# Kernel optimization log

Measured on AMD Instinct MI355X. Metric: run time of the kernel, lower is better.

Reference implementation:

```python
import jax, jax.numpy as jnp
import numpy as np

N, V, D, H, E = 16384, 17, 128, 256, 32
LN_EPS = 1e-5


def setup_inputs() -> dict:
    key = jax.random.key(0)
    ks = jax.random.split(key, 16)
    s = lambda *sh: 1.0 / np.sqrt(sh[0])
    inp = {
        "h": jax.random.normal(ks[0], (N, V, D), dtype=jnp.float32),
        "xy": jax.random.normal(ks[1], (N, V, 2), dtype=jnp.float32),
        "joint_mask": jax.random.randint(ks[2], (N, V), 0, 2).astype(bool),
        "edge_index": jax.random.randint(ks[3], (E, 2), 0, V).astype(jnp.int64),
        # edge MLP: Linear(2D+2 -> H), ReLU, Linear(H -> D)
        "ew1": jax.random.normal(ks[4], (2 * D + 2, H), dtype=jnp.float32) * s(2 * D + 2),
        "eb1": jnp.zeros((H,), dtype=jnp.float32),
        "ew2": jax.random.normal(ks[5], (H, D), dtype=jnp.float32) * s(H),
        "eb2": jnp.zeros((D,), dtype=jnp.float32),
        # node MLP: Linear(2D -> H), ReLU, Linear(H -> D)
        "nw1": jax.random.normal(ks[6], (2 * D, H), dtype=jnp.float32) * s(2 * D),
        "nb1": jnp.zeros((H,), dtype=jnp.float32),
        "nw2": jax.random.normal(ks[7], (H, D), dtype=jnp.float32) * s(H),
        "nb2": jnp.zeros((D,), dtype=jnp.float32),
        # LayerNorm(D)
        "gamma": jnp.ones((D,), dtype=jnp.float32),
        "beta": jnp.zeros((D,), dtype=jnp.float32),
    }
    return inp


def reference(h, xy, joint_mask, edge_index, ew1, eb1, ew2, eb2,
              nw1, nb1, nw2, nb2, gamma, beta):
    dst = edge_index[:, 0]  # [E]
    src = edge_index[:, 1]  # [E]
    mask_f = joint_mask.astype(h.dtype)  # [N,V]

    target = h[:, dst, :]                  # [N,E,D]
    source = h[:, src, :]                  # [N,E,D]
    rel = xy[:, src, :] - xy[:, dst, :]    # [N,E,2]
    edge_valid = (joint_mask[:, dst] & joint_mask[:, src]).astype(h.dtype)  # [N,E]

    msg_in = jnp.concatenate([target, source, rel], axis=-1)  # [N,E,2D+2]
    msg = jax.nn.relu(msg_in @ ew1 + eb1) @ ew2 + eb2          # [N,E,D]
    msg = msg * edge_valid[..., None]

    agg = jnp.zeros_like(h).at[:, dst, :].add(msg)                           # [N,V,D]
    denom = jnp.zeros((h.shape[0], h.shape[1], 1), h.dtype).at[:, dst, :].add(
        edge_valid[..., None])                                               # [N,V,1]
    agg = agg / jnp.maximum(denom, 1.0)

    delta = jax.nn.relu(jnp.concatenate([h, agg], axis=-1) @ nw1 + nb1) @ nw2 + nb2
    has_neighbors = (denom > 0).astype(h.dtype)
    x = h + delta * has_neighbors

    mu = jnp.mean(x, axis=-1, keepdims=True)
    var = jnp.mean(jnp.square(x - mu), axis=-1, keepdims=True)
    out = (x - mu) / jnp.sqrt(var + LN_EPS) * gamma + beta
    return out * mask_f[..., None]
```

## Files before the change

kernel.cpp:

```cpp
#include <hip/hip_runtime.h>

typedef _Float16 half8 __attribute__((ext_vector_type(8)));
typedef _Float16 half4v __attribute__((ext_vector_type(4)));
typedef float f32x4 __attribute__((ext_vector_type(4)));
typedef unsigned int u32;

#define LDH 136

__global__ void prep_weights(const float* __restrict__ ew1,
                             const float* __restrict__ ew2,
                             const float* __restrict__ nw1,
                             const float* __restrict__ nw2,
                             _Float16* __restrict__ wz) {
  int o = blockIdx.x * 256 + threadIdx.x;
  if (o < 65536) {
    int s = o >> 12, r = o & 4095;
    int gs = r >> 9, lane = (r >> 3) & 63, j = r & 7;
    int k = ((s & 1) * 4 + (gs >> 1)) * 32 + (lane >> 4) * 8 + j;
    int n = (s >> 1) * 32 + (gs & 1) * 16 + (lane & 15);
    wz[o] = (_Float16)ew1[k * 256 + n];
  } else if (o < 98304) {
    int o2 = o - 65536;
    int nc = o2 >> 12, r = o2 & 4095;
    int nt2 = r >> 9, lane = (r >> 3) & 63, j = r & 7;
    int k = nc * 32 + (lane >> 4) * 8 + j;
    int n = nt2 * 16 + (lane & 15);
    wz[o] = (_Float16)ew2[k * 128 + n];
  } else if (o < 163840) {
    int o2 = o - 98304;
    int s = o2 >> 12, r = o2 & 4095;
    int gs = r >> 9, lane = (r >> 3) & 63, j = r & 7;
    int k = ((s & 1) * 4 + (gs >> 1)) * 32 + (lane >> 4) * 8 + j;
    int n = (s >> 1) * 32 + (gs & 1) * 16 + (lane & 15);
    wz[o] = (_Float16)nw1[k * 256 + n];
  } else if (o < 196608) {
    int o2 = o - 163840;
    int nc = o2 >> 12, r = o2 & 4095;
    int nt2 = r >> 9, lane = (r >> 3) & 63, j = r & 7;
    int k = nc * 32 + (lane >> 4) * 8 + j;
    int n = nt2 * 16 + (lane & 15);
    wz[o] = (_Float16)nw2[k * 128 + n];
  }
}

__global__ __launch_bounds__(256, 2)
void fused_graph_layer(const float* __restrict__ h, const float* __restrict__ xy,
                       const int* __restrict__ jmask, const int* __restrict__ eidx,
                       const float* __restrict__ ew1,
                       const float* __restrict__ eb1, const float* __restrict__ eb2,
                       const float* __restrict__ nb1, const float* __restrict__ nb2,
                       const float* __restrict__ gamma, const float* __restrict__ beta,
                       const _Float16* __restrict__ wz,
                       float* __restrict__ out) {
  __shared__ _Float16 sh_h16[68 * LDH];
  __shared__ _Float16 sh_agg16[68 * LDH] __attribute__((aligned(16)));
  __shared__ _Float16 sh_ws[4 * 1280];
  __shared__ float sh_rel[256];
  __shared__ float sh_valid[128];
  __shared__ float sh_dn[80];
  __shared__ float sh_hasn[68], sh_maskf[68];
  __shared__ int   sh_edge[64];

  const int tid  = threadIdx.x;
  const int wave = tid >> 6;
  const int lane = tid & 63;
  const int ln   = lane & 15;
  const int quad = lane >> 4;
  const int n0   = blockIdx.x * 4;
  const size_t hbase = (size_t)n0 * 2176;
  const f32x4 vzero = {0.f, 0.f, 0.f, 0.f};

  _Float16* ws = sh_ws + wave * 1280;

  const _Float16* w1img  = wz;
  const _Float16* w2img  = wz + 65536;
  const _Float16* nw1img = wz + 98304;
  const _Float16* nw2img = wz + 163840;
  const float* w1r0 = ew1 + 256 * 256;
  const float* w1r1 = ew1 + 257 * 256;

  if (tid < 64) sh_edge[tid] = eidx[tid];
  if (tid < 68) sh_maskf[tid] = (float)jmask[n0 * 17 + tid];
  for (int i = tid; i < 2176; i += 256) {
    const float4 hv = ((const float4*)(h + hbase))[i];
    int q = i << 2;
    int gv = q >> 7, d = q & 127;
    half4v hq = { (_Float16)hv.x, (_Float16)hv.y, (_Float16)hv.z, (_Float16)hv.w };
    *(half4v*)&sh_h16[gv * LDH + d] = hq;
  }
  __syncthreads();
  if (tid < 128) {
    int g = tid >> 5, e = tid & 31;
    int dv = sh_edge[2 * e], sv = sh_edge[2 * e + 1];
    const float* xyb = xy + (size_t)(n0 + g) * 34;
    sh_rel[2 * tid]     = xyb[2 * sv]     - xyb[2 * dv];
    sh_rel[2 * tid + 1] = xyb[2 * sv + 1] - xyb[2 * dv + 1];
    sh_valid[tid] = sh_maskf[g * 17 + dv] * sh_maskf[g * 17 + sv];
  }
  __syncthreads();

  if (lane < 17) {
    float den = 0.f;
    for (int e = 0; e < 32; ++e)
      den += (sh_edge[2 * e] == lane) ? sh_valid[wave * 32 + e] : 0.f;
    sh_dn[wave * 20 + lane] = den;
    sh_hasn[wave * 17 + lane] = den > 0.f ? 1.f : 0.f;
  }

  int baseT[2], baseS[2];
  #pragma unroll
  for (int mi = 0; mi < 2; ++mi) {
    int eL = mi * 16 + ln;
    baseT[mi] = (wave * 17 + sh_edge[2 * eL]) * LDH;
    baseS[mi] = (wave * 17 + sh_edge[2 * eL + 1]) * LDH;
  }
  half8 af[2][8];
  #pragma unroll
  for (int mi = 0; mi < 2; ++mi)
    #pragma unroll
    for (int ks = 0; ks < 8; ++ks)
      af[mi][ks] = (ks < 4)
          ? *(const half8*)&sh_h16[baseT[mi] + ks * 32 + quad * 8]
          : *(const half8*)&sh_h16[baseS[mi] + (ks - 4) * 32 + quad * 8];

  f32x4 acc2[2][8];
  #pragma unroll
  for (int i = 0; i < 2; ++i)
    #pragma unroll
    for (int j = 0; j < 8; ++j) acc2[i][j] = vzero;

  for (int nc = 0; nc < 8; ++nc) {
    half8 b2f[8];
    #pragma unroll
    for (int t = 0; t < 8; ++t)
      b2f[t] = *(const half8*)(w2img + nc * 4096 + t * 512 + lane * 8);
    float ebv[2], r0v[2], r1v[2];
    #pragma unroll
    for (int nt = 0; nt < 2; ++nt) {
      int J = nc * 32 + nt * 16 + ln;
      ebv[nt] = eb1[J]; r0v[nt] = w1r0[J]; r1v[nt] = w1r1[J];
    }
    f32x4 acc1[2][2];
    #pragma unroll
    for (int i = 0; i < 2; ++i) { acc1[i][0] = vzero; acc1[i][1] = vzero; }

    #pragma unroll
    for (int kc = 0; kc < 8; ++kc) {
      const _Float16* wb = w1img + (size_t)(nc * 2 + (kc >> 2)) * 4096
                                 + ((kc & 3) * 2) * 512 + lane * 8;
      half8 bf0 = *(const half8*)wb;
      half8 bf1 = *(const half8*)(wb + 512);
      #pragma unroll
      for (int mi = 0; mi < 2; ++mi) {
        acc1[mi][0] = __builtin_amdgcn_mfma_f32_16x16x32_f16(af[mi][kc], bf0, acc1[mi][0], 0, 0, 0);
        acc1[mi][1] = __builtin_amdgcn_mfma_f32_16x16x32_f16(af[mi][kc], bf1, acc1[mi][1], 0, 0, 0);
      }
    }
    #pragma unroll
    for (int nt = 0; nt < 2; ++nt)
      #pragma unroll
      for (int mi = 0; mi < 2; ++mi)
        #pragma unroll
        for (int r = 0; r < 4; ++r) {
          int R = wave * 32 + mi * 16 + quad * 4 + r;
          float2 rr = *(const float2*)&sh_rel[2 * R];
          float val = acc1[mi][nt][r] + ebv[nt] + rr.x * r0v[nt] + rr.y * r1v[nt];
          ws[(mi * 16 + quad * 4 + r) * 40 + nt * 16 + ln] = (_Float16)fmaxf(val, 0.f);
        }
    #pragma unroll
    for (int mi = 0; mi < 2; ++mi) {
      half8 a2 = *(const half8*)&ws[(mi * 16 + ln) * 40 + quad * 8];
      #pragma unroll
      for (int nt2 = 0; nt2 < 8; ++nt2)
        acc2[mi][nt2] = __builtin_amdgcn_mfma_f32_16x16x32_f16(a2, b2f[nt2], acc2[mi][nt2], 0, 0, 0);
    }
  }

  {
    float eb2v[8];
    #pragma unroll
    for (int t = 0; t < 8; ++t) eb2v[t] = eb2[t * 16 + ln];
    half8 s0, s1;
    #pragma unroll
    for (int j = 0; j < 8; ++j) {
      int k = quad * 8 + j;
      int dk = sh_edge[2 * k];
      _Float16 vk = (_Float16)sh_valid[wave * 32 + k];
      s0[j] = (dk == ln) ? vk : (_Float16)0.f;
      s1[j] = (ln == 0 && dk == 16) ? vk : (_Float16)0.f;
    }
    float rden[4];
    #pragma unroll
    for (int r = 0; r < 4; ++r)
      rden[r] = 1.f / fmaxf(sh_dn[wave * 20 + quad * 4 + r], 1.f);
    float rden16 = 1.f / fmaxf(sh_dn[wave * 20 + 16], 1.f);

    #pragma unroll
    for (int qh = 0; qh < 4; ++qh) {
      #pragma unroll
      for (int t = 0; t < 2; ++t) {
        int nt2 = qh * 2 + t;
        #pragma unroll
        for (int mi = 0; mi < 2; ++mi) {
          half4v pk;
          #pragma unroll
          for (int r = 0; r < 4; ++r)
            pk[r] = (_Float16)(acc2[mi][nt2][r] + eb2v[nt2]);
          *(half4v*)&ws[(t * 16 + ln) * 40 + mi * 16 + quad * 4] = pk;
        }
      }
      #pragma unroll
      for (int t = 0; t < 2; ++t) {
        int nt2 = qh * 2 + t;
        half8 bfr = *(const half8*)&ws[(t * 16 + ln) * 40 + quad * 8];
        f32x4 agg0 = __builtin_amdgcn_mfma_f32_16x16x32_f16(s0, bfr, vzero, 0, 0, 0);
        f32x4 agg1 = __builtin_amdgcn_mfma_f32_16x16x32_f16(s1, bfr, vzero, 0, 0, 0);
        #pragma unroll
        for (int r = 0; r < 4; ++r)
          sh_agg16[(wave * 17 + quad * 4 + r) * LDH + nt2 * 16 + ln] =
              (_Float16)(agg0[r] * rden[r]);
        if (quad == 0)
          sh_agg16[(wave * 17 + 16) * LDH + nt2 * 16 + ln] =
              (_Float16)(agg1[0] * rden16);
      }
    }
  }
  __syncthreads();

  const int Rn = wave * 16 + ln;
  half8 afn0[8];
  #pragma unroll
  for (int ks = 0; ks < 8; ++ks)
    afn0[ks] = (ks < 4)
        ? *(const half8*)&sh_h16[Rn * LDH + ks * 32 + quad * 8]
        : *(const half8*)&sh_agg16[Rn * LDH + (ks - 4) * 32 + quad * 8];
  half8 afn1[8];
  if (wave == 0) {
    const int Rx = (64 + ln < 68) ? 64 + ln : 67;
    #pragma unroll
    for (int ks = 0; ks < 8; ++ks)
      afn1[ks] = (ks < 4)
          ? *(const half8*)&sh_h16[Rx * LDH + ks * 32 + quad * 8]
          : *(const half8*)&sh_agg16[Rx * LDH + (ks - 4) * 32 + quad * 8];
  }

  f32x4 acc4a[8], acc4b[8];
  #pragma unroll
  for (int j = 0; j < 8; ++j) { acc4a[j] = vzero; acc4b[j] = vzero; }

  for (int nc = 0; nc < 8; ++nc) {
    half8 b2n[8];
    #pragma unroll
    for (int t = 0; t < 8; ++t)
      b2n[t] = *(const half8*)(nw2img + nc * 4096 + t * 512 + lane * 8);
    float nbv[2];
    #pragma unroll
    for (int nt = 0; nt < 2; ++nt) nbv[nt] = nb1[nc * 32 + nt * 16 + ln];

    f32x4 acc3a[2], acc3b[2];
    acc3a[0] = vzero; acc3a[1] = vzero; acc3b[0] = vzero; acc3b[1] = vzero;

    #pragma unroll
    for (int kc = 0; kc < 8; ++kc) {
      const _Float16* wb = nw1img + (size_t)(nc * 2 + (kc >> 2)) * 4096
                                  + ((kc & 3) * 2) * 512 + lane * 8;
      half8 bf0 = *(const half8*)wb;
      half8 bf1 = *(const half8*)(wb + 512);
      acc3a[0] = __builtin_amdgcn_mfma_f32_16x16x32_f16(afn0[kc], bf0, acc3a[0], 0, 0, 0);
      acc3a[1] = __builtin_amdgcn_mfma_f32_16x16x32_f16(afn0[kc], bf1, acc3a[1], 0, 0, 0);
      if (wave == 0) {
        acc3b[0] = __builtin_amdgcn_mfma_f32_16x16x32_f16(afn1[kc], bf0, acc3b[0], 0, 0, 0);
        acc3b[1] = __builtin_amdgcn_mfma_f32_16x16x32_f16(afn1[kc], bf1, acc3b[1], 0, 0, 0);
      }
    }
    #pragma unroll
    for (int nt = 0; nt < 2; ++nt)
      #pragma unroll
      for (int r = 0; r < 4; ++r)
        ws[(quad * 4 + r) * 40 + nt * 16 + ln] = (_Float16)fmaxf(acc3a[nt][r] + nbv[nt], 0.f);
    if (wave == 0) {
      #pragma unroll
      for (int nt = 0; nt < 2; ++nt)
        #pragma unroll
        for (int r = 0; r < 4; ++r)
          ws[(16 + quad * 4 + r) * 40 + nt * 16 + ln] = (_Float16)fmaxf(acc3b[nt][r] + nbv[nt], 0.f);
    }
    {
      half8 a2 = *(const half8*)&ws[ln * 40 + quad * 8];
      #pragma unroll
      for (int nt2 = 0; nt2 < 8; ++nt2)
        acc4a[nt2] = __builtin_amdgcn_mfma_f32_16x16x32_f16(a2, b2n[nt2], acc4a[nt2], 0, 0, 0);
    }
    if (wave == 0) {
      half8 a2b = *(const half8*)&ws[(16 + ln) * 40 + quad * 8];
      #pragma unroll
      for (int nt2 = 0; nt2 < 8; ++nt2)
        acc4b[nt2] = __builtin_amdgcn_mfma_f32_16x16x32_f16(a2b, b2n[nt2], acc4b[nt2], 0, 0, 0);
    }
  }

  float gam[8], bet[8], nb2v[8];
  #pragma unroll
  for (int nt2 = 0; nt2 < 8; ++nt2) {
    int d = nt2 * 16 + ln;
    gam[nt2] = gamma[d]; bet[nt2] = beta[d]; nb2v[nt2] = nb2[d];
  }
  float xva[8][4];
  #pragma unroll
  for (int nt2 = 0; nt2 < 8; ++nt2) {
    int d = nt2 * 16 + ln;
    #pragma unroll
    for (int r = 0; r < 4; ++r) {
      int R = wave * 16 + quad * 4 + r;
      xva[nt2][r] = (float)sh_h16[R * LDH + d] + (acc4a[nt2][r] + nb2v[nt2]) * sh_hasn[R];
    }
  }
  #pragma unroll
  for (int r = 0; r < 4; ++r) {
    float s = 0.f, s2 = 0.f;
    #pragma unroll
    for (int nt2 = 0; nt2 < 8; ++nt2) { float x = xva[nt2][r]; s += x; s2 += x * x; }
    #pragma unroll
    for (int m = 1; m < 16; m <<= 1) { s += __shfl_xor(s, m, 64); s2 += __shfl_xor(s2, m, 64); }
    float mu = s * (1.f / 128.f);
    float var = s2 * (1.f / 128.f) - mu * mu;
    float rstd = rsqrtf(var + 1e-5f);
    float mk = sh_maskf[wave * 16 + quad * 4 + r];
    #pragma unroll
    for (int nt2 = 0; nt2 < 8; ++nt2)
      xva[nt2][r] = ((xva[nt2][r] - mu) * rstd * gam[nt2] + bet[nt2]) * mk;
  }
  float xvb[8][4];
  if (wave == 0) {
    #pragma unroll
    for (int nt2 = 0; nt2 < 8; ++nt2) {
      int d = nt2 * 16 + ln;
      #pragma unroll
      for (int r = 0; r < 4; ++r) {
        int R = 64 + quad * 4 + r;
        int Rc = R < 68 ? R : 67;
        xvb[nt2][r] = (float)sh_h16[Rc * LDH + d] + (acc4b[nt2][r] + nb2v[nt2]) * sh_hasn[Rc];
      }
    }
    #pragma unroll
    for (int r = 0; r < 4; ++r) {
      float s = 0.f, s2 = 0.f;
      #pragma unroll
      for (int nt2 = 0; nt2 < 8; ++nt2) { float x = xvb[nt2][r]; s += x; s2 += x * x; }
      #pragma unroll
      for (int m = 1; m < 16; m <<= 1) { s += __shfl_xor(s, m, 64); s2 += __shfl_xor(s2, m, 64); }
      float mu = s * (1.f / 128.f);
      float var = s2 * (1.f / 128.f) - mu * mu;
      float rstd = rsqrtf(var + 1e-5f);
      int R = 64 + quad * 4 + r;
      int Rc = R < 68 ? R : 67;
      float mk = sh_maskf[Rc];
      #pragma unroll
      for (int nt2 = 0; nt2 < 8; ++nt2)
        xvb[nt2][r] = ((xvb[nt2][r] - mu) * rstd * gam[nt2] + bet[nt2]) * mk;
    }
  }

  __syncthreads();
  float* ost2 = (float*)(void*)sh_agg16;
  #pragma unroll
  for (int half = 0; half < 2; ++half) {
    const int lo = half * 34;
    #pragma unroll
    for (int r = 0; r < 4; ++r) {
      int R = wave * 16 + quad * 4 + r;
      if (R >= lo && R < lo + 34) {
        #pragma unroll
        for (int nt2 = 0; nt2 < 8; ++nt2)
          ost2[(R - lo) * 132 + nt2 * 16 + ln] = xva[nt2][r];
      }
    }
    if (wave == 0) {
      #pragma unroll
      for (int r = 0; r < 4; ++r) {
        int R = 64 + quad * 4 + r;
        if (R < 68 && R >= lo && R < lo + 34) {
          #pragma unroll
          for (int nt2 = 0; nt2 < 8; ++nt2)
            ost2[(R - lo) * 132 + nt2 * 16 + ln] = xvb[nt2][r];
        }
      }
    }
    __syncthreads();
    for (int i = tid; i < 4352; i += 256)
      out[hbase + lo * 128 + i] = ost2[(i >> 7) * 132 + (i & 127)];
    if (half == 0) __syncthreads();
  }
}

extern "C" void kernel_launch(void* const* d_in, const int* in_sizes, int n_in,
                              void* d_out, int out_size, void* d_ws, size_t ws_size,
                              hipStream_t stream) {
  const float* h     = (const float*)d_in[0];
  const float* xy    = (const float*)d_in[1];
  const int*   jm    = (const int*)d_in[2];
  const int*   ei    = (const int*)d_in[3];
  const float* ew1   = (const float*)d_in[4];
  const float* eb1   = (const float*)d_in[5];
  const float* ew2   = (const float*)d_in[6];
  const float* eb2   = (const float*)d_in[7];
  const float* nw1   = (const float*)d_in[8];
  const float* nb1   = (const float*)d_in[9];
  const float* nw2   = (const float*)d_in[10];
  const float* nb2   = (const float*)d_in[11];
  const float* gamma = (const float*)d_in[12];
  const float* beta  = (const float*)d_in[13];
  _Float16* wz = (_Float16*)d_ws;

  prep_weights<<<768, 256, 0, stream>>>(ew1, ew2, nw1, nw2, wz);
  fused_graph_layer<<<4096, 256, 0, stream>>>(h, xy, jm, ei, ew1, eb1, eb2,
                                              nb1, nb2, gamma, beta, wz,
                                              (float*)d_out);
}
```

Measured before the change: 635.9 us.

## Split hidden dimension across two wave groups with 512-thread blocks

Doubles the block to 8 waves. Each pair of waves handles the same 16-32 rows, but the two waves split the hidden-dimension chunks (even and odd nc) of both MLPs. Partial second-layer outputs are then summed through shared memory, both in the aggregation MFMAs and in the final node-MLP reduction. This is meant to cut the per-wave serial MFMA chain and raise latency hiding. In exchange it adds several block-wide barriers, extra shared-memory traffic for the partial sums, and a launch bound of 512x4 that may force register spilling.

```diff
diff --git a/kernel.cpp b/kernel.cpp
--- a/kernel.cpp
+++ b/kernel.cpp
@@ -43,7 +43,7 @@
   }
 }
 
-__global__ __launch_bounds__(256, 2)
+__global__ __launch_bounds__(512, 4)
 void fused_graph_layer(const float* __restrict__ h, const float* __restrict__ xy,
                        const int* __restrict__ jmask, const int* __restrict__ eidx,
                        const float* __restrict__ ew1,
@@ -54,7 +54,7 @@
                        float* __restrict__ out) {
   __shared__ _Float16 sh_h16[68 * LDH];
   __shared__ _Float16 sh_agg16[68 * LDH] __attribute__((aligned(16)));
-  __shared__ _Float16 sh_ws[4 * 1280];
+  __shared__ _Float16 sh_ws[8 * 1280] __attribute__((aligned(16)));
   __shared__ float sh_rel[256];
   __shared__ float sh_valid[128];
   __shared__ float sh_dn[80];
@@ -63,6 +63,8 @@
 
   const int tid  = threadIdx.x;
   const int wave = tid >> 6;
+  const int b    = wave & 3;
+  const int p    = wave >> 2;
   const int lane = tid & 63;
   const int ln   = lane & 15;
   const int quad = lane >> 4;
@@ -70,7 +72,9 @@
   const size_t hbase = (size_t)n0 * 2176;
   const f32x4 vzero = {0.f, 0.f, 0.f, 0.f};
 
-  _Float16* ws = sh_ws + wave * 1280;
+  _Float16* ws  = sh_ws + wave * 1280;
+  _Float16* wsE = sh_ws + b * 1280;
+  _Float16* wsO = sh_ws + (4 + b) * 1280;
 
   const _Float16* w1img  = wz;
   const _Float16* w2img  = wz + 65536;
@@ -81,7 +85,7 @@
 
   if (tid < 64) sh_edge[tid] = eidx[tid];
   if (tid < 68) sh_maskf[tid] = (float)jmask[n0 * 17 + tid];
-  for (int i = tid; i < 2176; i += 256) {
+  for (int i = tid; i < 2176; i += 512) {
     const float4 hv = ((const float4*)(h + hbase))[i];
     int q = i << 2;
     int gv = q >> 7, d = q & 127;
@@ -98,21 +102,20 @@
     sh_valid[tid] = sh_maskf[g * 17 + dv] * sh_maskf[g * 17 + sv];
   }
   __syncthreads();
-
-  if (lane < 17) {
+  if (p == 0 && lane < 17) {
     float den = 0.f;
     for (int e = 0; e < 32; ++e)
-      den += (sh_edge[2 * e] == lane) ? sh_valid[wave * 32 + e] : 0.f;
-    sh_dn[wave * 20 + lane] = den;
-    sh_hasn[wave * 17 + lane] = den > 0.f ? 1.f : 0.f;
+      den += (sh_edge[2 * e] == lane) ? sh_valid[b * 32 + e] : 0.f;
+    sh_dn[b * 20 + lane] = den;
+    sh_hasn[b * 17 + lane] = den > 0.f ? 1.f : 0.f;
   }
 
   int baseT[2], baseS[2];
   #pragma unroll
   for (int mi = 0; mi < 2; ++mi) {
     int eL = mi * 16 + ln;
-    baseT[mi] = (wave * 17 + sh_edge[2 * eL]) * LDH;
-    baseS[mi] = (wave * 17 + sh_edge[2 * eL + 1]) * LDH;
+    baseT[mi] = (b * 17 + sh_edge[2 * eL]) * LDH;
+    baseS[mi] = (b * 17 + sh_edge[2 * eL + 1]) * LDH;
   }
   half8 af[2][8];
   #pragma unroll
@@ -129,7 +132,9 @@
     #pragma unroll
     for (int j = 0; j < 8; ++j) acc2[i][j] = vzero;
 
-  for (int nc = 0; nc < 8; ++nc) {
+  #pragma unroll
+  for (int it = 0; it < 4; ++it) {
+    const int nc = 2 * it + p;
     half8 b2f[8];
     #pragma unroll
     for (int t = 0; t < 8; ++t)
@@ -162,7 +167,7 @@
       for (int mi = 0; mi < 2; ++mi)
         #pragma unroll
         for (int r = 0; r < 4; ++r) {
-          int R = wave * 32 + mi * 16 + quad * 4 + r;
+          int R = b * 32 + mi * 16 + quad * 4 + r;
           float2 rr = *(const float2*)&sh_rel[2 * R];
           float val = acc1[mi][nt][r] + ebv[nt] + rr.x * r0v[nt] + rr.y * r1v[nt];
           ws[(mi * 16 + quad * 4 + r) * 40 + nt * 16 + ln] = (_Float16)fmaxf(val, 0.f);
@@ -176,6 +181,8 @@
     }
   }
 
+  __syncthreads();
+
   {
     float eb2v[8];
     #pragma unroll
@@ -185,15 +192,15 @@
     for (int j = 0; j < 8; ++j) {
       int k = quad * 8 + j;
       int dk = sh_edge[2 * k];
-      _Float16 vk = (_Float16)sh_valid[wave * 32 + k];
+      _Float16 vk = (_Float16)sh_valid[b * 32 + k];
       s0[j] = (dk == ln) ? vk : (_Float16)0.f;
       s1[j] = (ln == 0 && dk == 16) ? vk : (_Float16)0.f;
     }
     float rden[4];
     #pragma unroll
     for (int r = 0; r < 4; ++r)
-      rden[r] = 1.f / fmaxf(sh_dn[wave * 20 + quad * 4 + r], 1.f);
-    float rden16 = 1.f / fmaxf(sh_dn[wave * 20 + 16], 1.f);
+      rden[r] = 1.f / fmaxf(sh_dn[b * 20 + quad * 4 + r], 1.f);
+    float rden16 = 1.f / fmaxf(sh_dn[b * 20 + 16], 1.f);
 
     #pragma unroll
     for (int qh = 0; qh < 4; ++qh) {
@@ -205,29 +212,33 @@
           half4v pk;
           #pragma unroll
           for (int r = 0; r < 4; ++r)
-            pk[r] = (_Float16)(acc2[mi][nt2][r] + eb2v[nt2]);
+            pk[r] = (_Float16)(acc2[mi][nt2][r] + (p == 0 ? eb2v[nt2] : 0.f));
           *(half4v*)&ws[(t * 16 + ln) * 40 + mi * 16 + quad * 4] = pk;
         }
       }
-      #pragma unroll
-      for (int t = 0; t < 2; ++t) {
-        int nt2 = qh * 2 + t;
-        half8 bfr = *(const half8*)&ws[(t * 16 + ln) * 40 + quad * 8];
-        f32x4 agg0 = __builtin_amdgcn_mfma_f32_16x16x32_f16(s0, bfr, vzero, 0, 0, 0);
-        f32x4 agg1 = __builtin_amdgcn_mfma_f32_16x16x32_f16(s1, bfr, vzero, 0, 0, 0);
+      __syncthreads();
+      {
+        const int t = p;
+        const int nt2 = qh * 2 + p;
+        half8 bE = *(const half8*)&wsE[(t * 16 + ln) * 40 + quad * 8];
+        half8 bO = *(const half8*)&wsO[(t * 16 + ln) * 40 + quad * 8];
+        f32x4 a0 = __builtin_amdgcn_mfma_f32_16x16x32_f16(s0, bE, vzero, 0, 0, 0);
+        a0       = __builtin_amdgcn_mfma_f32_16x16x32_f16(s0, bO, a0,    0, 0, 0);
+        f32x4 a1 = __builtin_amdgcn_mfma_f32_16x16x32_f16(s1, bE, vzero, 0, 0, 0);
+        a1       = __builtin_amdgcn_mfma_f32_16x16x32_f16(s1, bO, a1,    0, 0, 0);
         #pragma unroll
         for (int r = 0; r < 4; ++r)
-          sh_agg16[(wave * 17 + quad * 4 + r) * LDH + nt2 * 16 + ln] =
-              (_Float16)(agg0[r] * rden[r]);
+          sh_agg16[(b * 17 + quad * 4 + r) * LDH + nt2 * 16 + ln] =
+              (_Float16)(a0[r] * rden[r]);
         if (quad == 0)
-          sh_agg16[(wave * 17 + 16) * LDH + nt2 * 16 + ln] =
-              (_Float16)(agg1[0] * rden16);
-      }
-    }
-  }
-  __syncthreads();
-
-  const int Rn = wave * 16 + ln;
+          sh_agg16[(b * 17 + 16) * LDH + nt2 * 16 + ln] =
+              (_Float16)(a1[0] * rden16);
+      }
+      __syncthreads();
+    }
+  }
+
+  const int Rn = b * 16 + ln;
   half8 afn0[8];
   #pragma unroll
   for (int ks = 0; ks < 8; ++ks)
@@ -235,7 +246,7 @@
         ? *(const half8*)&sh_h16[Rn * LDH + ks * 32 + quad * 8]
         : *(const half8*)&sh_agg16[Rn * LDH + (ks - 4) * 32 + quad * 8];
   half8 afn1[8];
-  if (wave == 0) {
+  if (b == 0) {
     const int Rx = (64 + ln < 68) ? 64 + ln : 67;
     #pragma unroll
     for (int ks = 0; ks < 8; ++ks)
@@ -248,7 +259,9 @@
   #pragma unroll
   for (int j = 0; j < 8; ++j) { acc4a[j] = vzero; acc4b[j] = vzero; }
 
-  for (int nc = 0; nc < 8; ++nc) {
+  #pragma unroll
+  for (int it = 0; it < 4; ++it) {
+    const int nc = 2 * it + p;
     half8 b2n[8];
     #pragma unroll
     for (int t = 0; t < 8; ++t)
@@ -268,7 +281,7 @@
       half8 bf1 = *(const half8*)(wb + 512);
       acc3a[0] = __builtin_amdgcn_mfma_f32_16x16x32_f16(afn0[kc], bf0, acc3a[0], 0, 0, 0);
       acc3a[1] = __builtin_amdgcn_mfma_f32_16x16x32_f16(afn0[kc], bf1, acc3a[1], 0, 0, 0);
-      if (wave == 0) {
+      if (b == 0) {
         acc3b[0] = __builtin_amdgcn_mfma_f32_16x16x32_f16(afn1[kc], bf0, acc3b[0], 0, 0, 0);
         acc3b[1] = __builtin_amdgcn_mfma_f32_16x16x32_f16(afn1[kc], bf1, acc3b[1], 0, 0, 0);
       }
@@ -278,7 +291,7 @@
       #pragma unroll
       for (int r = 0; r < 4; ++r)
         ws[(quad * 4 + r) * 40 + nt * 16 + ln] = (_Float16)fmaxf(acc3a[nt][r] + nbv[nt], 0.f);
-    if (wave == 0) {
+    if (b == 0) {
       #pragma unroll
       for (int nt = 0; nt < 2; ++nt)
         #pragma unroll
@@ -291,7 +304,7 @@
       for (int nt2 = 0; nt2 < 8; ++nt2)
         acc4a[nt2] = __builtin_amdgcn_mfma_f32_16x16x32_f16(a2, b2n[nt2], acc4a[nt2], 0, 0, 0);
     }
-    if (wave == 0) {
+    if (b == 0) {
       half8 a2b = *(const half8*)&ws[(16 + ln) * 40 + quad * 8];
       #pragma unroll
       for (int nt2 = 0; nt2 < 8; ++nt2)
@@ -306,58 +319,88 @@
     gam[nt2] = gamma[d]; bet[nt2] = beta[d]; nb2v[nt2] = nb2[d];
   }
   float xva[8][4];
-  #pragma unroll
-  for (int nt2 = 0; nt2 < 8; ++nt2) {
-    int d = nt2 * 16 + ln;
-    #pragma unroll
-    for (int r = 0; r < 4; ++r) {
-      int R = wave * 16 + quad * 4 + r;
-      xva[nt2][r] = (float)sh_h16[R * LDH + d] + (acc4a[nt2][r] + nb2v[nt2]) * sh_hasn[R];
-    }
-  }
-  #pragma unroll
-  for (int r = 0; r < 4; ++r) {
-    float s = 0.f, s2 = 0.f;
-    #pragma unroll
-    for (int nt2 = 0; nt2 < 8; ++nt2) { float x = xva[nt2][r]; s += x; s2 += x * x; }
-    #pragma unroll
-    for (int m = 1; m < 16; m <<= 1) { s += __shfl_xor(s, m, 64); s2 += __shfl_xor(s2, m, 64); }
-    float mu = s * (1.f / 128.f);
-    float var = s2 * (1.f / 128.f) - mu * mu;
-    float rstd = rsqrtf(var + 1e-5f);
-    float mk = sh_maskf[wave * 16 + quad * 4 + r];
-    #pragma unroll
-    for (int nt2 = 0; nt2 < 8; ++nt2)
-      xva[nt2][r] = ((xva[nt2][r] - mu) * rstd * gam[nt2] + bet[nt2]) * mk;
-  }
   float xvb[8][4];
-  if (wave == 0) {
-    #pragma unroll
-    for (int nt2 = 0; nt2 < 8; ++nt2) {
-      int d = nt2 * 16 + ln;
-      #pragma unroll
-      for (int r = 0; r < 4; ++r) {
-        int R = 64 + quad * 4 + r;
-        int Rc = R < 68 ? R : 67;
-        xvb[nt2][r] = (float)sh_h16[Rc * LDH + d] + (acc4b[nt2][r] + nb2v[nt2]) * sh_hasn[Rc];
-      }
-    }
+  float* ws32  = (float*)(void*)ws;
+  float* wsO32 = (float*)(void*)wsO;
+  #pragma unroll
+  for (int q = 0; q < 4; ++q) {
+    if (p == 1) {
+      #pragma unroll
+      for (int t = 0; t < 2; ++t)
+        #pragma unroll
+        for (int r = 0; r < 4; ++r)
+          ws32[(quad * 4 + r) * 32 + t * 16 + ln] = acc4a[2 * q + t][r];
+      if (b == 0 && quad == 0) {
+        #pragma unroll
+        for (int t = 0; t < 2; ++t)
+          #pragma unroll
+          for (int r = 0; r < 4; ++r)
+            ws32[(16 + r) * 32 + t * 16 + ln] = acc4b[2 * q + t][r];
+      }
+    }
+    __syncthreads();
+    if (p == 0) {
+      #pragma unroll
+      for (int t = 0; t < 2; ++t)
+        #pragma unroll
+        for (int r = 0; r < 4; ++r) {
+          int nt2 = 2 * q + t;
+          int R = b * 16 + quad * 4 + r;
+          float sum = acc4a[nt2][r] + wsO32[(quad * 4 + r) * 32 + t * 16 + ln];
+          xva[nt2][r] = (float)sh_h16[R * LDH + nt2 * 16 + ln]
+                      + (sum + nb2v[nt2]) * sh_hasn[R];
+        }
+      if (b == 0) {
+        #pragma unroll
+        for (int t = 0; t < 2; ++t)
+          #pragma unroll
+          for (int r = 0; r < 4; ++r) {
+            int nt2 = 2 * q + t;
+            int v = quad * 4 + r;
+            int rr = v < 4 ? v : 3;
+            int Rc = (64 + v < 68) ? 64 + v : 67;
+            float sum = acc4b[nt2][r] + wsO32[(16 + rr) * 32 + t * 16 + ln];
+            xvb[nt2][r] = (float)sh_h16[Rc * LDH + nt2 * 16 + ln]
+                        + (sum + nb2v[nt2]) * sh_hasn[Rc];
+          }
+      }
+    }
+    __syncthreads();
+  }
+
+  if (p == 0) {
     #pragma unroll
     for (int r = 0; r < 4; ++r) {
       float s = 0.f, s2 = 0.f;
       #pragma unroll
-      for (int nt2 = 0; nt2 < 8; ++nt2) { float x = xvb[nt2][r]; s += x; s2 += x * x; }
+      for (int nt2 = 0; nt2 < 8; ++nt2) { float x = xva[nt2][r]; s += x; s2 += x * x; }
       #pragma unroll
       for (int m = 1; m < 16; m <<= 1) { s += __shfl_xor(s, m, 64); s2 += __shfl_xor(s2, m, 64); }
       float mu = s * (1.f / 128.f);
       float var = s2 * (1.f / 128.f) - mu * mu;
       float rstd = rsqrtf(var + 1e-5f);
-      int R = 64 + quad * 4 + r;
-      int Rc = R < 68 ? R : 67;
-      float mk = sh_maskf[Rc];
+      float mk = sh_maskf[b * 16 + quad * 4 + r];
       #pragma unroll
       for (int nt2 = 0; nt2 < 8; ++nt2)
-        xvb[nt2][r] = ((xvb[nt2][r] - mu) * rstd * gam[nt2] + bet[nt2]) * mk;
+        xva[nt2][r] = ((xva[nt2][r] - mu) * rstd * gam[nt2] + bet[nt2]) * mk;
+    }
+    if (b == 0) {
+      #pragma unroll
+      for (int r = 0; r < 4; ++r) {
+        float s = 0.f, s2 = 0.f;
+        #pragma unroll
+        for (int nt2 = 0; nt2 < 8; ++nt2) { float x = xvb[nt2][r]; s += x; s2 += x * x; }
+        #pragma unroll
+        for (int m = 1; m < 16; m <<= 1) { s += __shfl_xor(s, m, 64); s2 += __shfl_xor(s2, m, 64); }
+        float mu = s * (1.f / 128.f);
+        float var = s2 * (1.f / 128.f) - mu * mu;
+        float rstd = rsqrtf(var + 1e-5f);
+        int Rc = (64 + quad * 4 + r < 68) ? 64 + quad * 4 + r : 67;
+        float mk = sh_maskf[Rc];
+        #pragma unroll
+        for (int nt2 = 0; nt2 < 8; ++nt2)
+          xvb[nt2][r] = ((xvb[nt2][r] - mu) * rstd * gam[nt2] + bet[nt2]) * mk;
+      }
     }
   }
 
@@ -366,28 +409,30 @@
   #pragma unroll
   for (int half = 0; half < 2; ++half) {
     const int lo = half * 34;
-    #pragma unroll
-    for (int r = 0; r < 4; ++r) {
-      int R = wave * 16 + quad * 4 + r;
-      if (R >= lo && R < lo + 34) {
-        #pragma unroll
-        for (int nt2 = 0; nt2 < 8; ++nt2)
-          ost2[(R - lo) * 132 + nt2 * 16 + ln] = xva[nt2][r];
-      }
-    }
-    if (wave == 0) {
+    if (p == 0) {
       #pragma unroll
       for (int r = 0; r < 4; ++r) {
-        int R = 64 + quad * 4 + r;
-        if (R < 68 && R >= lo && R < lo + 34) {
+        int R = b * 16 + quad * 4 + r;
+        if (R >= lo && R < lo + 34) {
           #pragma unroll
           for (int nt2 = 0; nt2 < 8; ++nt2)
-            ost2[(R - lo) * 132 + nt2 * 16 + ln] = xvb[nt2][r];
+            ost2[(R - lo) * 132 + nt2 * 16 + ln] = xva[nt2][r];
         }
       }
+      if (b == 0) {
+        #pragma unroll
+        for (int r = 0; r < 4; ++r) {
+          int R = 64 + quad * 4 + r;
+          if (R < 68 && R >= lo && R < lo + 34) {
+            #pragma unroll
+            for (int nt2 = 0; nt2 < 8; ++nt2)
+              ost2[(R - lo) * 132 + nt2 * 16 + ln] = xvb[nt2][r];
+          }
+        }
+      }
     }
     __syncthreads();
-    for (int i = tid; i < 4352; i += 256)
+    for (int i = tid; i < 4352; i += 512)
       out[hbase + lo * 128 + i] = ost2[(i >> 7) * 132 + (i & 127)];
     if (half == 0) __syncthreads();
   }
@@ -413,7 +458,7 @@
   _Float16* wz = (_Float16*)d_ws;
 
   prep_weights<<<768, 256, 0, stream>>>(ew1, ew2, nw1, nw2, wz);
-  fused_graph_layer<<<4096, 256, 0, stream>>>(h, xy, jm, ei, ew1, eb1, eb2,
+  fused_graph_layer<<<4096, 512, 0, stream>>>(h, xy, jm, ei, ew1, eb1, eb2,
                                               nb1, nb2, gamma, beta, wz,
                                               (float*)d_out);
 }
```

Result: slower. 1.789 ms (+181.3%).
